# Performance work log

Measured on AMD Instinct MI355X. Metric: run time of the kernel, lower is better.

## Reference

```python
import jax, jax.numpy as jnp
import numpy as np

D_MODEL = 1024; D_STATE = 64; D_CONV = 7; EXPAND = 2; HEADDIM = 64; NGROUPS = 1
D_INNER = EXPAND * D_MODEL            # 2048
NHEADS = D_INNER // HEADDIM           # 32
D_IN_PROJ = 2 * D_INNER + 2 * (2 * NGROUPS * D_STATE) + 2 * NHEADS  # 4416
CONV_DIM = D_INNER + 2 * (2 * NGROUPS * D_STATE)                     # 2304
BATCH = 2; SEQLEN = 2048
EPS = 1e-5


def setup_inputs() -> dict:
    key = jax.random.key(0)
    ks = jax.random.split(key, 8)
    u = jax.random.normal(ks[0], (BATCH, SEQLEN, D_MODEL), jnp.float32)
    W_in = jax.random.normal(ks[1], (D_IN_PROJ, D_MODEL), jnp.float32) * 0.02
    conv_w = jax.random.normal(ks[2], (CONV_DIM, 1, D_CONV), jnp.float32) * 0.2
    conv_b = jax.random.normal(ks[3], (CONV_DIM,), jnp.float32) * 0.02
    # dt_bias init as in module: inv-softplus of dt sampled log-uniform in [dt_min, dt_max]
    dt = jnp.exp(jax.random.uniform(ks[4], (NHEADS,)) * (np.log(0.1) - np.log(0.001)) + np.log(0.001))
    dt = jnp.clip(dt, 1e-4)
    dt_bias = dt + jnp.log(-jnp.expm1(-dt))
    A_log = jnp.zeros((NHEADS,), jnp.float32)          # A = -exp(A_log) = -1
    Dp = jnp.ones((NHEADS,), jnp.float32)
    fc_D_w = jax.random.normal(ks[5], (NHEADS, D_INNER), jnp.float32) * 0.02
    norm_w = jnp.ones((D_INNER,), jnp.float32)
    W_out = jax.random.normal(ks[6], (D_MODEL, D_INNER), jnp.float32) * 0.02
    return dict(u=u, W_in=W_in, conv_w=conv_w, conv_b=conv_b, dt_bias=dt_bias,
                A_log=A_log, Dp=Dp, fc_D_w=fc_D_w, norm_w=norm_w, W_out=W_out)


def reference(u, W_in, conv_w, conv_b, dt_bias, A_log, Dp, fc_D_w, norm_w, W_out):
    b, L, _ = u.shape
    gn = NGROUPS * D_STATE
    zxbcdt = jnp.einsum('bld,ed->ble', u, W_in)              # (b,L,4416)
    A = -jnp.exp(A_log)                                       # (H,)
    z = zxbcdt[..., :D_INNER]
    xBC = zxbcdt[..., D_INNER:D_INNER + CONV_DIM]
    dt_raw = zxbcdt[..., D_INNER + CONV_DIM:]                 # (b,L,2H)
    # fwd dt + time-flipped bwd dt stacked along batch -> (2b,L,H)
    dt = jnp.concatenate([dt_raw[..., :NHEADS], dt_raw[..., NHEADS:][:, ::-1]], axis=0)
    dt = jax.nn.softplus(dt + dt_bias)                        # dt_limit=(0,inf): softplus already >= 0
    # depthwise conv1d, 'same' padding
    xc = jnp.transpose(xBC, (0, 2, 1))                        # (b,Cd,L)
    xc = jax.lax.conv_general_dilated(xc, conv_w, (1,), [(D_CONV // 2, D_CONV // 2)],
                                      dimension_numbers=('NCH', 'OIH', 'NCH'),
                                      feature_group_count=CONV_DIM)
    xc = xc + conv_b[None, :, None]
    xBC = jax.nn.silu(jnp.transpose(xc, (0, 2, 1)))           # (b,L,Cd)
    x = xBC[..., :D_INNER]
    BC = xBC[..., D_INNER:]
    x_og = x
    x2 = jnp.concatenate([x, x[:, ::-1]], axis=0)             # (2b,L,d_inner)
    BC2 = jnp.concatenate([BC[..., :2 * gn], BC[..., 2 * gn:][:, ::-1]], axis=0)
    Bm = BC2[..., :gn].reshape(2 * b, L, NGROUPS, D_STATE)
    Cm = BC2[..., gn:].reshape(2 * b, L, NGROUPS, D_STATE)
    x_scan = x2.reshape(2 * b, L, NHEADS, HEADDIM)
    hpg = NHEADS // NGROUPS
    Bh = jnp.repeat(Bm, hpg, axis=2)                          # (2b,L,H,N)
    Ch = jnp.repeat(Cm, hpg, axis=2)

    def step(state, ins):                                     # state: (2b,H,P,N)
        x_t, dt_t, B_t, C_t = ins
        ex = jnp.exp(A[None, :, None, None] * dt_t[:, :, None, None])
        state = state * ex + x_t[..., None] * B_t[:, :, None, :]
        y_t = jnp.sum(state * C_t[:, :, None, :], axis=-1)    # (2b,H,P)
        return state, y_t

    xs = (jnp.moveaxis(x_scan, 1, 0), jnp.moveaxis(dt, 1, 0),
          jnp.moveaxis(Bh, 1, 0), jnp.moveaxis(Ch, 1, 0))
    state0 = jnp.zeros((2 * b, NHEADS, HEADDIM, D_STATE), u.dtype)
    _, ys = jax.lax.scan(step, state0, xs)                    # (L,2b,H,P)
    y = jnp.moveaxis(ys, 0, 1).reshape(2 * b, L, D_INNER)
    # shift_right: drop last step, zero at t=0
    y = jnp.concatenate([jnp.zeros_like(y[:, :1]), y[:, :-1]], axis=1)
    y_fw, y_bw = y[:b], y[b:][:, ::-1]
    diag_heads = jnp.einsum('bld,hd->blh', x_og, fc_D_w) + Dp # fc_D(x_og) with bias D
    diag = jnp.repeat(diag_heads, HEADDIM, axis=-1)           # expand per-head -> d_inner
    y = y_fw + y_bw + x_og * diag
    # RMSNormGated (norm before gate)
    rms = jnp.sqrt(jnp.mean(y * y, axis=-1, keepdims=True) + EPS)
    y = norm_w * (y / rms) * jax.nn.silu(z)
    return jnp.einsum('ble,de->bld', y, W_out)
```

## Files before the change

### kernel.cpp

```cpp
#include <hip/hip_runtime.h>
#include <cstdint>
#include <cstddef>

#define L_SEQ   2048
#define DMODEL  1024
#define DINNER  2048
#define NHEADS_ 32
#define HEADDIM_ 64
#define DSTATE  64
#define CONVDIM 2304
#define DINPROJ 4416
#define DINPROJ_P 4608
#define BATCH_  2
#define EPS_    1e-5f
#define PITCH   72
#define KSPL    8

typedef __attribute__((ext_vector_type(8))) short bf16x8;
typedef __attribute__((ext_vector_type(4))) float f32x4;
typedef unsigned short ushort_t;
typedef unsigned int uint_t;
typedef __attribute__((address_space(3))) unsigned int as3_uint;
typedef __attribute__((address_space(1))) const unsigned int as1_uint;

__device__ __forceinline__ float silu_f(float v) { return v / (1.f + __expf(-v)); }
__device__ __forceinline__ ushort_t f2bf(float f) {
    uint_t u = __float_as_uint(f);
    return (ushort_t)((u + 0x7FFFu + ((u >> 16) & 1u)) >> 16);
}
__device__ __forceinline__ float bf2f(ushort_t u) {
    return __uint_as_float(((uint_t)u) << 16);
}
__device__ __forceinline__ void gload16(const void* g, void* l) {
    __builtin_amdgcn_global_load_lds((as1_uint*)g, (as3_uint*)l, 16, 0, 0);
}

#define N0U ((size_t)(4096 * 1024 / 4))
#define N1U ((size_t)(DINPROJ_P * DMODEL / 4))
#define N2U ((size_t)(DMODEL * DINNER / 4))
#define N3U ((size_t)(64 * DINNER / 4))
__global__ __launch_bounds__(256)
void cvt_all(const float* __restrict__ u, const float* __restrict__ W_in,
             const float* __restrict__ W_out, const float* __restrict__ fcD,
             ushort_t* __restrict__ ubf, ushort_t* __restrict__ wibf,
             ushort_t* __restrict__ wobf, ushort_t* __restrict__ fcdbf) {
    size_t unit = (size_t)blockIdx.x * 256 + threadIdx.x;
    if (unit >= N0U + N1U + N2U + N3U) return;
    const float* src; ushort_t* dst; size_t i4; bool zero = false;
    if (unit < N0U) {
        i4 = unit; src = u; dst = ubf;
    } else if (unit < N0U + N1U) {
        i4 = unit - N0U; src = W_in; dst = wibf;
        zero = ((int)(i4 / (DMODEL / 4)) >= DINPROJ);
    } else if (unit < N0U + N1U + N2U) {
        i4 = unit - N0U - N1U; src = W_out; dst = wobf;
    } else {
        i4 = unit - N0U - N1U - N2U; src = fcD; dst = fcdbf;
        zero = ((int)(i4 / (DINNER / 4)) >= NHEADS_);
    }
    float4 v = zero ? make_float4(0.f, 0.f, 0.f, 0.f)
                    : reinterpret_cast<const float4*>(src)[i4];
    ushort_t* d = dst + i4 * 4;
    d[0] = f2bf(v.x); d[1] = f2bf(v.y); d[2] = f2bf(v.z); d[3] = f2bf(v.w);
}

__global__ __launch_bounds__(512, 2)
void gemm_8ph(const ushort_t* __restrict__ Ap, const ushort_t* __restrict__ Bp,
              ushort_t* __restrict__ Cbf, int M, int N, int K, int nbn) {
    const int nwg = gridDim.x;
    const int orig = blockIdx.x;
    const int xcd = orig & 7, q_ = nwg >> 3, r_ = nwg & 7;
    const int wg = ((xcd < r_) ? (xcd * (q_ + 1)) : (r_ * (q_ + 1) + (xcd - r_) * q_)) + (orig >> 3);
    const int bm = (wg / nbn) * 256, bn = (wg % nbn) * 256;

    __shared__ __align__(16) char smem[131072];

    const int tid = threadIdx.x;
    const int wave = tid >> 6, lane = tid & 63;
    const int wr = wave >> 2, wc = wave & 3;
    const int fr = lane & 15, kg = lane >> 4, rg = lane >> 4;

    const ushort_t* gptr[8]; uint_t glds[8];
#pragma unroll
    for (int i = 0; i < 8; ++i) {
        int unit = i >> 1, g = i & 1;
        int isB = unit & 1, half = unit >> 1;
        int rbase = half * 128 + wave * 16 + g * 8;
        int rl = rbase + (lane >> 3);
        int slot = (lane & 7) ^ (lane >> 3);
        gptr[i] = (isB ? Bp : Ap) + (size_t)((isB ? bn : bm) + rl) * (size_t)K + slot * 8;
        glds[i] = (uint_t)(isB * 32768 + rbase * 128);
    }
    auto stage = [&](int pbuf, int t) {
#pragma unroll
        for (int i = 0; i < 8; ++i)
            gload16(gptr[i] + (size_t)t * 64, smem + pbuf * 65536 + glds[i]);
    };

    f32x4 acc[8][4];
#pragma unroll
    for (int m = 0; m < 8; ++m)
#pragma unroll
        for (int n = 0; n < 4; ++n) acc[m][n] = (f32x4){0.f, 0.f, 0.f, 0.f};

    bf16x8 aF[4][2];
    bf16x8 bF[2][2][2];

    auto lda_frag = [&](int pbuf, int mh) {
#pragma unroll
        for (int mm = 0; mm < 4; ++mm)
#pragma unroll
            for (int kk = 0; kk < 2; ++kk) {
                int Rl = wr * 128 + mh * 64 + mm * 16 + fr;
                aF[mm][kk] = *reinterpret_cast<const bf16x8*>(
                    smem + pbuf * 65536 + Rl * 128 + (((kk * 4 + kg) ^ (Rl & 7)) << 4));
            }
    };
    auto ldb_frag = [&](int pbuf, int nh) {
#pragma unroll
        for (int nn = 0; nn < 2; ++nn)
#pragma unroll
            for (int kk = 0; kk < 2; ++kk) {
                int Rl = wc * 64 + (nh * 2 + nn) * 16 + fr;
                bF[nh][nn][kk] = *reinterpret_cast<const bf16x8*>(
                    smem + pbuf * 65536 + 32768 + Rl * 128 + (((kk * 4 + kg) ^ (Rl & 7)) << 4));
            }
    };
    auto do_mfma = [&](int mh, int nh) {
        __builtin_amdgcn_s_setprio(1);
#pragma unroll
        for (int mm = 0; mm < 4; ++mm)
#pragma unroll
            for (int nn = 0; nn < 2; ++nn)
#pragma unroll
                for (int kk = 0; kk < 2; ++kk)
                    acc[mh * 4 + mm][nh * 2 + nn] = __builtin_amdgcn_mfma_f32_16x16x32_bf16(
                        aF[mm][kk], bF[nh][nn][kk], acc[mh * 4 + mm][nh * 2 + nn], 0, 0, 0);
        __builtin_amdgcn_s_setprio(0);
    };

    const int NT = K / 64;
    stage(0, 0);
    asm volatile("s_waitcnt vmcnt(0)" ::: "memory");
    __builtin_amdgcn_sched_barrier(0);
    __builtin_amdgcn_s_barrier();

    for (int t = 0; t < NT; ++t) {
        const int p = t & 1;
        if (t + 1 < NT) stage(p ^ 1, t + 1);
        if (t > 0) {
            if (t + 1 < NT) asm volatile("s_waitcnt vmcnt(8)" ::: "memory");
            else            asm volatile("s_waitcnt vmcnt(0)" ::: "memory");
            __builtin_amdgcn_sched_barrier(0);
        }
        __builtin_amdgcn_s_barrier();
        lda_frag(p, 0); ldb_frag(p, 0);
        asm volatile("s_waitcnt lgkmcnt(0)" ::: "memory");
        __builtin_amdgcn_sched_barrier(0);
        do_mfma(0, 0);
        __builtin_amdgcn_s_barrier();
        ldb_frag(p, 1);
        asm volatile("s_waitcnt lgkmcnt(0)" ::: "memory");
        __builtin_amdgcn_sched_barrier(0);
        do_mfma(0, 1);
        __builtin_amdgcn_s_barrier();
        lda_frag(p, 1);
        asm volatile("s_waitcnt lgkmcnt(0)" ::: "memory");
        __builtin_amdgcn_sched_barrier(0);
        do_mfma(1, 0);
        __builtin_amdgcn_s_barrier();
        do_mfma(1, 1);
        __builtin_amdgcn_s_barrier();
    }

    char* ct = smem;
#pragma unroll
    for (int m = 0; m < 8; ++m)
#pragma unroll
        for (int n = 0; n < 4; ++n) {
#pragma unroll
            for (int r = 0; r < 4; ++r) {
                int lr = wr * 128 + m * 16 + rg * 4 + r;
                int lc = wc * 64 + n * 16 + fr;
                int byte = lr * 512 + ((lc * 2) ^ ((lr & 7) << 4));
                *reinterpret_cast<ushort_t*>(ct + byte) = f2bf(acc[m][n][r]);
            }
        }
    __syncthreads();
    for (int pass = 0; pass < 16; ++pass) {
        int unit = pass * 512 + tid;
        int row = unit >> 5, u = unit & 31;
        uint4 v = *reinterpret_cast<const uint4*>(ct + row * 512 + ((u * 16) ^ ((row & 7) << 4)));
        *reinterpret_cast<uint4*>(&Cbf[(size_t)(bm + row) * N + bn + u * 8]) = v;
    }
}

template<int BM, int BN, int WGM, int WGN, int FM, int FN, int MODE>
__global__ __launch_bounds__(256)
void gemm_nt_mfma(const ushort_t* __restrict__ A, const ushort_t* __restrict__ B,
                  float* __restrict__ C, ushort_t* __restrict__ Cbf,
                  int M, int N, int K, int lda, int ldb, int nbn) {
    const int nwg = gridDim.x;
    const int orig = blockIdx.x;
    const int xcd = orig & 7, q = nwg >> 3, r = nwg & 7;
    const int wg = ((xcd < r) ? (xcd * (q + 1)) : (r * (q + 1) + (xcd - r) * q)) + (orig >> 3);

    int bm, bn, kbeg, kend, ks = 0;
    if (MODE == 2) {
        bm = (wg / nbn) * BM; bn = 0; ks = wg % nbn;
        kbeg = ks * (K / nbn); kend = kbeg + K / nbn;
    } else {
        bm = (wg / nbn) * BM; bn = (wg % nbn) * BN;
        kbeg = 0; kend = K;
    }

    constexpr int BUFSZ = (BM + BN) * 64;
    constexpr int EPI_B = (MODE == 2) ? 0 : BM * 256;
    constexpr int SMEM_B = (2 * BUFSZ > EPI_B) ? 2 * BUFSZ : EPI_B;
    __shared__ __align__(16) char smem[SMEM_B];

    const int tid = threadIdx.x;
    const int wave = tid >> 6, lane = tid & 63;
    const int wr = wave / WGN, wc = wave % WGN;
    const int fr = lane & 15, kg = lane >> 4;

    constexpr int AI = BM / 64, BI = BN / 64;
    size_t aoff[AI]; int aLds[AI];
#pragma unroll
    for (int pp = 0; pp < AI; ++pp) {
        int p = wave * AI + pp;
        int row = p * 16 + (lane >> 2);
        int c16 = (lane & 3) ^ ((row >> 1) & 3);
        aoff[pp] = (size_t)(bm + row) * lda + c16 * 8;
        aLds[pp] = p * 1024;
    }
    size_t boff[BI]; int bLds[BI];
#pragma unroll
    for (int pp = 0; pp < BI; ++pp) {
        int p = wave * BI + pp;
        int row = p * 16 + (lane >> 2);
        int c16 = (lane & 3) ^ ((row >> 1) & 3);
        boff[pp] = (size_t)(bn + row) * ldb + c16 * 8;
        bLds[pp] = BM * 64 + p * 1024;
    }

    auto stage = [&](int buf, int k0) {
        char* bp = smem + buf * BUFSZ;
#pragma unroll
        for (int pp = 0; pp < AI; ++pp) gload16(&A[aoff[pp] + k0], bp + aLds[pp]);
#pragma unroll
        for (int pp = 0; pp < BI; ++pp) gload16(&B[boff[pp] + k0], bp + bLds[pp]);
    };

    f32x4 acc[FM][FN];
#pragma unroll
    for (int m = 0; m < FM; ++m)
#pragma unroll
        for (int n = 0; n < FN; ++n) acc[m][n] = (f32x4){0.f, 0.f, 0.f, 0.f};

    stage(0, kbeg);
    __syncthreads();

    const int NT = (kend - kbeg) / 32;
    for (int t = 0; t < NT; ++t) {
        const int cur = t & 1;
        if (t + 1 < NT) stage(cur ^ 1, kbeg + (t + 1) * 32);

        const char* bp = smem + cur * BUFSZ;
        bf16x8 af[FM], bfv[FN];
#pragma unroll
        for (int m = 0; m < FM; ++m) {
            int row = wr * FM * 16 + m * 16 + fr;
            af[m] = *reinterpret_cast<const bf16x8*>(bp + row * 64 + ((kg ^ ((row >> 1) & 3)) << 4));
        }
#pragma unroll
        for (int n = 0; n < FN; ++n) {
            int row = wc * FN * 16 + n * 16 + fr;
            bfv[n] = *reinterpret_cast<const bf16x8*>(bp + BM * 64 + row * 64 + ((kg ^ ((row >> 1) & 3)) << 4));
        }
#pragma unroll
        for (int m = 0; m < FM; ++m)
#pragma unroll
            for (int n = 0; n < FN; ++n)
                acc[m][n] = __builtin_amdgcn_mfma_f32_16x16x32_bf16(af[m], bfv[n], acc[m][n], 0, 0, 0);
        __syncthreads();
    }

    const int rg = lane >> 4;
    if (MODE == 2) {
        float* Cp = C + (size_t)ks * M * NHEADS_;
#pragma unroll
        for (int m = 0; m < FM; ++m)
#pragma unroll
            for (int n = 0; n < FN; ++n) {
                int col = wc * FN * 16 + n * 16 + fr;
#pragma unroll
                for (int r = 0; r < 4; ++r) {
                    int rowg = bm + wr * FM * 16 + m * 16 + rg * 4 + r;
                    if (col < NHEADS_) Cp[(size_t)rowg * NHEADS_ + col] = acc[m][n][r];
                }
            }
    } else {
        char* ct = smem;
#pragma unroll
        for (int m = 0; m < FM; ++m)
#pragma unroll
            for (int n = 0; n < FN; ++n) {
#pragma unroll
                for (int r = 0; r < 4; ++r) {
                    int lr = wr * FM * 16 + m * 16 + rg * 4 + r;
                    int lc = wc * FN * 16 + n * 16 + fr;
                    int byte = (lr * 256 + lc * 4) ^ ((lr & 7) << 4);
                    *reinterpret_cast<float*>(ct + byte) = acc[m][n][r];
                }
            }
        __syncthreads();
        const int lrow = tid >> 4, seg16 = (tid & 15) * 16;
#pragma unroll
        for (int j = 0; j < BM / 16; ++j) {
            int lr = j * 16 + lrow;
            uint4 v = *reinterpret_cast<const uint4*>(ct + ((lr * 256 + seg16) ^ ((lr & 7) << 4)));
            *reinterpret_cast<uint4*>(&C[(size_t)(bm + lr) * N + bn + seg16 / 4]) = v;
        }
    }
}

__global__ __launch_bounds__(256)
void conv_kernel(const ushort_t* __restrict__ zxbf, const float* __restrict__ conv_w,
                 const float* __restrict__ conv_b, ushort_t* __restrict__ xBCbf) {
    const int c = blockIdx.x * 256 + threadIdx.x;
    const int t0 = blockIdx.y * 16;
    const int beta = blockIdx.z;
    float w[7];
#pragma unroll
    for (int k = 0; k < 7; ++k) w[k] = conv_w[c * 7 + k];
    const float bias = conv_b[c];
    const ushort_t* in = zxbf + (size_t)beta * L_SEQ * DINPROJ_P + DINNER + c;
    float win[7];
#pragma unroll
    for (int j = 0; j < 6; ++j) {
        int t = t0 - 3 + j;
        win[j] = (t >= 0 && t < L_SEQ) ? bf2f(in[(size_t)t * DINPROJ_P]) : 0.f;
    }
    for (int i = 0; i < 16; ++i) {
        int t = t0 + i;
        int tl = t + 3;
        win[6] = (tl < L_SEQ) ? bf2f(in[(size_t)tl * DINPROJ_P]) : 0.f;
        float acc = bias;
#pragma unroll
        for (int k = 0; k < 7; ++k) acc += win[k] * w[k];
        xBCbf[((size_t)beta * L_SEQ + t) * CONVDIM + c] = f2bf(silu_f(acc));
#pragma unroll
        for (int j = 0; j < 6; ++j) win[j] = win[j + 1];
    }
}

__global__ __launch_bounds__(256)
void dtla_kernel(const ushort_t* __restrict__ zxbf, const float* __restrict__ dt_bias,
                 const float* __restrict__ A_log, float* __restrict__ labuf) {
    const int idx = blockIdx.x * 256 + threadIdx.x;
    const int h   = idx & 31;
    const int tau = (idx >> 5) & (L_SEQ - 1);
    const int bd  = idx >> 16;
    const int dir = bd >> 1, beta = bd & 1;
    const int tt  = dir ? (L_SEQ - 1 - tau) : tau;
    const float dtraw = bf2f(zxbf[((size_t)beta * L_SEQ + tt) * DINPROJ_P + DINNER + CONVDIM + dir * NHEADS_ + h]);
    const float Ah = -__expf(A_log[h]);
    const float dtv = dtraw + dt_bias[h];
    const float sp = (dtv > 15.f) ? dtv : log1pf(__expf(dtv));
    labuf[((size_t)bd * NHEADS_ + h) * L_SEQ + tau] = Ah * sp;
}

__global__ __launch_bounds__(256)
void ssd_chunk_kernel(const ushort_t* __restrict__ xBCbf, const float* __restrict__ labuf,
                      float* __restrict__ Pbuf, ushort_t* __restrict__ sdel,
                      ushort_t* __restrict__ yfw, ushort_t* __restrict__ ybw) {
    const int c  = blockIdx.x;
    const int h  = blockIdx.y;
    const int bd = blockIdx.z;
    const int dir = bd >> 1, beta = bd & 1;
    const int tid = threadIdx.x;
    const int wave = tid >> 6, lane = tid & 63;
    const int wr = wave >> 1, wc = wave & 1;
    const int fr = lane & 15, kg = lane >> 4, rg = lane >> 4;

    __shared__ short Bs[64 * PITCH], Cs[64 * PITCH], XTs[64 * PITCH],
                     BTs[64 * PITCH], Ms[64 * PITCH];
    __shared__ float lslds[64];

    const int row = tid >> 2, seg = tid & 3;
    const int tau_r = c * 64 + row;
    const int tt = dir ? (L_SEQ - 1 - tau_r) : tau_r;
    const ushort_t* gbase = xBCbf + ((size_t)beta * L_SEQ + tt) * CONVDIM;

    union U4 { uint4 v; ushort_t s[8]; };
    U4 x0, x1, b0, b1, c0, c1;
    x0.v = *reinterpret_cast<const uint4*>(gbase + h * 64 + seg * 16);
    x1.v = *reinterpret_cast<const uint4*>(gbase + h * 64 + seg * 16 + 8);
    b0.v = *reinterpret_cast<const uint4*>(gbase + DINNER + dir * 128 + seg * 16);
    b1.v = *reinterpret_cast<const uint4*>(gbase + DINNER + dir * 128 + seg * 16 + 8);
    c0.v = *reinterpret_cast<const uint4*>(gbase + DINNER + dir * 128 + 64 + seg * 16);
    c1.v = *reinterpret_cast<const uint4*>(gbase + DINNER + dir * 128 + 64 + seg * 16 + 8);

    *reinterpret_cast<uint4*>(&Bs[row * PITCH + seg * 16])     = b0.v;
    *reinterpret_cast<uint4*>(&Bs[row * PITCH + seg * 16 + 8]) = b1.v;
    *reinterpret_cast<uint4*>(&Cs[row * PITCH + seg * 16])     = c0.v;
    *reinterpret_cast<uint4*>(&Cs[row * PITCH + seg * 16 + 8]) = c1.v;
#pragma unroll
    for (int k = 0; k < 8; ++k) {
        XTs[(seg * 16 + k) * PITCH + row]     = x0.s[k];
        XTs[(seg * 16 + 8 + k) * PITCH + row] = x1.s[k];
    }

    if (tid < 64) {
        float v = labuf[((size_t)bd * NHEADS_ + h) * L_SEQ + c * 64 + tid];
#pragma unroll
        for (int d = 1; d < 64; d <<= 1) {
            float t = __shfl_up(v, d);
            if (lane >= d) v += t;
        }
        lslds[tid] = v;
        Pbuf[((size_t)bd * NHEADS_ + h) * L_SEQ + c * 64 + tid] = __expf(v);
    }
    __syncthreads();

    {
        const float wrow = __expf(lslds[63] - lslds[row]);
#pragma unroll
        for (int k = 0; k < 8; ++k) {
            BTs[(seg * 16 + k) * PITCH + row]     = (short)f2bf(bf2f(b0.s[k]) * wrow);
            BTs[(seg * 16 + 8 + k) * PITCH + row] = (short)f2bf(bf2f(b1.s[k]) * wrow);
        }
    }

    f32x4 accg[2][2];
#pragma unroll
    for (int mi = 0; mi < 2; ++mi)
#pragma unroll
        for (int nj = 0; nj < 2; ++nj) accg[mi][nj] = (f32x4){0.f, 0.f, 0.f, 0.f};
#pragma unroll
    for (int s = 0; s < 2; ++s) {
        int koff = kg * 8 + s * 32;
        bf16x8 af[2], bfv[2];
#pragma unroll
        for (int mi = 0; mi < 2; ++mi)
            af[mi] = *reinterpret_cast<const bf16x8*>(&Cs[(wr * 32 + mi * 16 + fr) * PITCH + koff]);
#pragma unroll
        for (int nj = 0; nj < 2; ++nj)
            bfv[nj] = *reinterpret_cast<const bf16x8*>(&Bs[(wc * 32 + nj * 16 + fr) * PITCH + koff]);
#pragma unroll
        for (int mi = 0; mi < 2; ++mi)
#pragma unroll
            for (int nj = 0; nj < 2; ++nj)
                accg[mi][nj] = __builtin_amdgcn_mfma_f32_16x16x32_bf16(af[mi], bfv[nj], accg[mi][nj], 0, 0, 0);
    }

#pragma unroll
    for (int mi = 0; mi < 2; ++mi)
#pragma unroll
        for (int nj = 0; nj < 2; ++nj) {
            int j = wc * 32 + nj * 16 + fr;
            float lsj = lslds[j];
#pragma unroll
            for (int r = 0; r < 4; ++r) {
                int i = wr * 32 + mi * 16 + rg * 4 + r;
                float v = accg[mi][nj][r];
                v = (i >= j) ? v * __expf(lslds[i] - lsj) : 0.f;
                Ms[i * PITCH + j] = (short)f2bf(v);
            }
        }
    __syncthreads();

    f32x4 accy[2][2], accs[2][2];
#pragma unroll
    for (int mi = 0; mi < 2; ++mi)
#pragma unroll
        for (int nj = 0; nj < 2; ++nj) {
            accy[mi][nj] = (f32x4){0.f, 0.f, 0.f, 0.f};
            accs[mi][nj] = (f32x4){0.f, 0.f, 0.f, 0.f};
        }
#pragma unroll
    for (int s = 0; s < 2; ++s) {
        int koff = kg * 8 + s * 32;
        bf16x8 am[2], axt[2], bxt[2], bbt[2];
#pragma unroll
        for (int mi = 0; mi < 2; ++mi) {
            am[mi]  = *reinterpret_cast<const bf16x8*>(&Ms[(wr * 32 + mi * 16 + fr) * PITCH + koff]);
            axt[mi] = *reinterpret_cast<const bf16x8*>(&XTs[(wr * 32 + mi * 16 + fr) * PITCH + koff]);
        }
#pragma unroll
        for (int nj = 0; nj < 2; ++nj) {
            bxt[nj] = *reinterpret_cast<const bf16x8*>(&XTs[(wc * 32 + nj * 16 + fr) * PITCH + koff]);
            bbt[nj] = *reinterpret_cast<const bf16x8*>(&BTs[(wc * 32 + nj * 16 + fr) * PITCH + koff]);
        }
#pragma unroll
        for (int mi = 0; mi < 2; ++mi)
#pragma unroll
            for (int nj = 0; nj < 2; ++nj) {
                accy[mi][nj] = __builtin_amdgcn_mfma_f32_16x16x32_bf16(am[mi], bxt[nj], accy[mi][nj], 0, 0, 0);
                accs[mi][nj] = __builtin_amdgcn_mfma_f32_16x16x32_bf16(axt[mi], bbt[nj], accs[mi][nj], 0, 0, 0);
            }
    }

    ushort_t* Yt = (ushort_t*)Bs;
    ushort_t* St = (ushort_t*)Cs;
#pragma unroll
    for (int mi = 0; mi < 2; ++mi)
#pragma unroll
        for (int nj = 0; nj < 2; ++nj) {
#pragma unroll
            for (int r = 0; r < 4; ++r) {
                int i  = wr * 32 + mi * 16 + rg * 4 + r;
                int jd = wc * 32 + nj * 16 + fr;
                St[i * 64 + jd] = f2bf(accs[mi][nj][r]);
                Yt[i * 64 + jd] = f2bf(accy[mi][nj][r]);
            }
        }
    __syncthreads();

    ushort_t* yout = dir ? ybw : yfw;
    ushort_t* sdp = sdel + (((size_t)bd * NHEADS_ + h) * 32 + c) * 4096;
    for (int un = tid; un < 512; un += 256) {
        const int rowi = un >> 3, ch = un & 7;
        uint4 sv = *reinterpret_cast<const uint4*>(St + rowi * 64 + ch * 8);
        *reinterpret_cast<uint4*>(sdp + rowi * 64 + ch * 8) = sv;
        uint4 yv = *reinterpret_cast<const uint4*>(Yt + rowi * 64 + ch * 8);
        int tau = c * 64 + rowi;
        int tout;
        if (tau == L_SEQ - 1) { tout = dir ? (L_SEQ - 1) : 0; yv = make_uint4(0, 0, 0, 0); }
        else                  { tout = dir ? (L_SEQ - 2 - tau) : (tau + 1); }
        *reinterpret_cast<uint4*>(yout + ((size_t)beta * L_SEQ + tout) * DINNER + h * 64 + ch * 8) = yv;
    }
}

__global__ __launch_bounds__(256)
void ssd_scan_kernel(const float* __restrict__ Pbuf, ushort_t* __restrict__ sdel) {
    const int bh = blockIdx.x;
    const int qt = blockIdx.y;
    const int eo = qt * 1024 + threadIdx.x * 4;
    ushort_t* base = sdel + (size_t)bh * 32 * 4096;
    const float* Pb = Pbuf + (size_t)bh * L_SEQ;

    float S0 = 0.f, S1 = 0.f, S2 = 0.f, S3 = 0.f;
    uint2 d = *reinterpret_cast<const uint2*>(base + eo);
    for (int c = 0; c < 32; ++c) {
        uint2 dn;
        if (c + 1 < 32) dn = *reinterpret_cast<const uint2*>(base + (size_t)(c + 1) * 4096 + eo);
        const float ptot = Pb[c * 64 + 63];
        uint2 pv;
        pv.x = (uint_t)f2bf(S0) | ((uint_t)f2bf(S1) << 16);
        pv.y = (uint_t)f2bf(S2) | ((uint_t)f2bf(S3) << 16);
        *reinterpret_cast<uint2*>(base + (size_t)c * 4096 + eo) = pv;
        S0 = ptot * S0 + bf2f((ushort_t)(d.x & 0xFFFF));
        S1 = ptot * S1 + bf2f((ushort_t)(d.x >> 16));
        S2 = ptot * S2 + bf2f((ushort_t)(d.y & 0xFFFF));
        S3 = ptot * S3 + bf2f((ushort_t)(d.y >> 16));
        d = dn;
    }
}

__global__ __launch_bounds__(256)
void ssd_yinter_kernel(const ushort_t* __restrict__ xBCbf, const float* __restrict__ Pbuf,
                       const ushort_t* __restrict__ sin_buf,
                       ushort_t* __restrict__ yfw, ushort_t* __restrict__ ybw) {
    const int c  = blockIdx.x;
    const int h  = blockIdx.y;
    const int bd = blockIdx.z;
    const int dir = bd >> 1, beta = bd & 1;
    const int tid = threadIdx.x;
    const int wave = tid >> 6, lane = tid & 63;
    const int fr = lane & 15, kg = lane >> 4, rg = lane >> 4;
    const int i0 = wave * 16;

    __shared__ short Cs[64 * PITCH], Ss[64 * PITCH];
    __shared__ float Pl[64];

    const int row = tid >> 2, seg = tid & 3;
    {
        const int tau_r = c * 64 + row;
        const int tt = dir ? (L_SEQ - 1 - tau_r) : tau_r;
        const ushort_t* gbase = xBCbf + ((size_t)beta * L_SEQ + tt) * CONVDIM + DINNER + dir * 128 + 64;
        uint4 cv0 = *reinterpret_cast<const uint4*>(gbase + seg * 16);
        uint4 cv1 = *reinterpret_cast<const uint4*>(gbase + seg * 16 + 8);
        *reinterpret_cast<uint4*>(&Cs[row * PITCH + seg * 16])     = cv0;
        *reinterpret_cast<uint4*>(&Cs[row * PITCH + seg * 16 + 8]) = cv1;
    }
    {
        const ushort_t* sb = sin_buf + (((size_t)bd * NHEADS_ + h) * 32 + c) * 4096;
        for (int un = tid; un < 512; un += 256) {
            const int ri = un >> 3, ch = un & 7;
            uint4 v = *reinterpret_cast<const uint4*>(sb + ri * 64 + ch * 8);
            *reinterpret_cast<uint4*>(&Ss[ri * PITCH + ch * 8]) = v;
        }
    }
    if (tid < 64) Pl[tid] = Pbuf[((size_t)bd * NHEADS_ + h) * L_SEQ + c * 64 + tid];
    __syncthreads();

    f32x4 accy[4];
#pragma unroll
    for (int nf = 0; nf < 4; ++nf) accy[nf] = (f32x4){0.f, 0.f, 0.f, 0.f};
#pragma unroll
    for (int s = 0; s < 2; ++s) {
        int koff = kg * 8 + s * 32;
        bf16x8 af = *reinterpret_cast<const bf16x8*>(&Cs[(i0 + fr) * PITCH + koff]);
#pragma unroll
        for (int nf = 0; nf < 4; ++nf) {
            bf16x8 bfv = *reinterpret_cast<const bf16x8*>(&Ss[(nf * 16 + fr) * PITCH + koff]);
            accy[nf] = __builtin_amdgcn_mfma_f32_16x16x32_bf16(af, bfv, accy[nf], 0, 0, 0);
        }
    }
    __syncthreads();

    ushort_t* Yt = (ushort_t*)Cs;
#pragma unroll
    for (int nf = 0; nf < 4; ++nf) {
        int hdl = nf * 16 + fr;
#pragma unroll
        for (int r = 0; r < 4; ++r) {
            int i = i0 + rg * 4 + r;
            Yt[i * 64 + hdl] = f2bf(accy[nf][r] * Pl[i]);
        }
    }
    __syncthreads();

    ushort_t* yout = dir ? ybw : yfw;
    for (int un = tid; un < 512; un += 256) {
        const int ri = un >> 3, ch = un & 7;
        int tau = c * 64 + ri;
        if (tau == L_SEQ - 1) continue;
        int tout = dir ? (L_SEQ - 2 - tau) : (tau + 1);
        ushort_t* gp = yout + ((size_t)beta * L_SEQ + tout) * DINNER + h * 64 + ch * 8;
        union U4 { uint4 v; ushort_t s[8]; } yo, cv, res;
        yo.v = *reinterpret_cast<const uint4*>(gp);
        cv.v = *reinterpret_cast<const uint4*>(Yt + ri * 64 + ch * 8);
#pragma unroll
        for (int k = 0; k < 8; ++k) res.s[k] = f2bf(bf2f(yo.s[k]) + bf2f(cv.s[k]));
        *reinterpret_cast<uint4*>(gp) = res.v;
    }
}

__global__ __launch_bounds__(256)
void combine_rms(const ushort_t* __restrict__ yfw, const ushort_t* __restrict__ ybw,
                 const ushort_t* __restrict__ xBCbf, const float* __restrict__ dpart,
                 const float* __restrict__ Dp,
                 const ushort_t* __restrict__ zxbf, const float* __restrict__ norm_w,
                 ushort_t* __restrict__ ybf) {
    const int row = blockIdx.x;
    const int tid = threadIdx.x;
    union U4 { uint4 v; ushort_t s[8]; };
    U4 yf, yb, xv, zv;
    yf.v = *reinterpret_cast<const uint4*>(yfw + (size_t)row * DINNER + tid * 8);
    yb.v = *reinterpret_cast<const uint4*>(ybw + (size_t)row * DINNER + tid * 8);
    xv.v = *reinterpret_cast<const uint4*>(xBCbf + (size_t)row * CONVDIM + tid * 8);
    zv.v = *reinterpret_cast<const uint4*>(zxbf + (size_t)row * DINPROJ_P + tid * 8);
    const int hh = tid >> 3;
    float dgv = Dp[hh];
#pragma unroll
    for (int ks = 0; ks < KSPL; ++ks)
        dgv += dpart[((size_t)ks * (BATCH_ * L_SEQ) + row) * NHEADS_ + hh];
    float v[8];
    float ss = 0.f;
#pragma unroll
    for (int i = 0; i < 8; ++i) {
        float val = bf2f(yf.s[i]) + bf2f(yb.s[i]) + bf2f(xv.s[i]) * dgv;
        v[i] = val;
        ss += val * val;
    }
    ss += __shfl_xor(ss, 1);  ss += __shfl_xor(ss, 2);  ss += __shfl_xor(ss, 4);
    ss += __shfl_xor(ss, 8);  ss += __shfl_xor(ss, 16); ss += __shfl_xor(ss, 32);
    __shared__ float wsum[4];
    if ((tid & 63) == 0) wsum[tid >> 6] = ss;
    __syncthreads();
    ss = wsum[0] + wsum[1] + wsum[2] + wsum[3];
    const float inv = rsqrtf(ss * (1.f / DINNER) + EPS_);
    U4 outv;
#pragma unroll
    for (int i = 0; i < 8; ++i) {
        int c = tid * 8 + i;
        outv.s[i] = f2bf(norm_w[c] * v[i] * inv * silu_f(bf2f(zv.s[i])));
    }
    *reinterpret_cast<uint4*>(ybf + (size_t)row * DINNER + tid * 8) = outv.v;
}

extern "C" void kernel_launch(void* const* d_in, const int* in_sizes, int n_in,
                              void* d_out, int out_size, void* d_ws, size_t ws_size,
                              hipStream_t stream) {
    const float* u       = (const float*)d_in[0];
    const float* W_in    = (const float*)d_in[1];
    const float* conv_w  = (const float*)d_in[2];
    const float* conv_b  = (const float*)d_in[3];
    const float* dt_bias = (const float*)d_in[4];
    const float* A_log   = (const float*)d_in[5];
    const float* Dp      = (const float*)d_in[6];
    const float* fc_D_w  = (const float*)d_in[7];
    const float* norm_w  = (const float*)d_in[8];
    const float* W_out   = (const float*)d_in[9];
    float* out = (float*)d_out;

    const int ROWS = BATCH_ * L_SEQ;
    ushort_t* zxbf  = (ushort_t*)d_ws;
    ushort_t* xBCbf = zxbf  + (size_t)ROWS * DINPROJ_P;
    ushort_t* yfw   = xBCbf + (size_t)ROWS * CONVDIM;
    ushort_t* ybw   = yfw   + (size_t)ROWS * DINNER;
    float* dpart = (float*)(ybw + (size_t)ROWS * DINNER);
    float* labuf = dpart + (size_t)KSPL * ROWS * NHEADS_;
    float* Pbuf  = labuf + (size_t)4 * NHEADS_ * L_SEQ;
    ushort_t* sdel = (ushort_t*)(Pbuf + (size_t)4 * NHEADS_ * L_SEQ);
    ushort_t* wobf = sdel + (size_t)4 * NHEADS_ * 32 * 64 * 64;
    ushort_t* fcdbf = wobf + (size_t)DMODEL * DINNER;
    ushort_t* ubf  = fcdbf + (size_t)64 * DINNER;
    ushort_t* wibf = ubf  + (size_t)ROWS * DMODEL;
    ushort_t* ybf  = ubf;

    const size_t total_units = N0U + N1U + N2U + N3U;
    cvt_all<<<(int)((total_units + 255) / 256), 256, 0, stream>>>(
        u, W_in, W_out, fc_D_w, ubf, wibf, wobf, fcdbf);

    gemm_8ph<<<(ROWS / 256) * (DINPROJ_P / 256), 512, 0, stream>>>(
        ubf, wibf, zxbf, ROWS, DINPROJ_P, DMODEL, DINPROJ_P / 256);

    dim3 gc(CONVDIM / 256, L_SEQ / 16, BATCH_);
    conv_kernel<<<gc, 256, 0, stream>>>(zxbf, conv_w, conv_b, xBCbf);

    dtla_kernel<<<(4 * L_SEQ * NHEADS_) / 256, 256, 0, stream>>>(zxbf, dt_bias, A_log, labuf);

    dim3 ga(32, NHEADS_, 4);
    ssd_chunk_kernel<<<ga, 256, 0, stream>>>(xBCbf, labuf, Pbuf, sdel, yfw, ybw);

    dim3 gsn(4 * NHEADS_, 4);
    ssd_scan_kernel<<<gsn, 256, 0, stream>>>(Pbuf, sdel);

    dim3 gy(32, NHEADS_, 4);
    ssd_yinter_kernel<<<gy, 256, 0, stream>>>(xBCbf, Pbuf, sdel, yfw, ybw);

    gemm_nt_mfma<64, 64, 2, 2, 2, 2, 2><<<(ROWS / 64) * KSPL, 256, 0, stream>>>(
        xBCbf, fcdbf, dpart, nullptr, ROWS, 64, DINNER, CONVDIM, DINNER, KSPL);

    combine_rms<<<ROWS, 256, 0, stream>>>(yfw, ybw, xBCbf, dpart, Dp, zxbf, norm_w, ybf);

    gemm_nt_mfma<128, 64, 2, 2, 4, 2, 0><<<(ROWS / 128) * (DMODEL / 64), 256, 0, stream>>>(
        ybf, wobf, out, nullptr, ROWS, DMODEL, DINNER, DINNER, DINNER, DMODEL / 64);
}
```

Measured before the change: 219.6 us.

## Interleave half-tile global loads with MFMA phases in the bf16 GEMM

Replaces the whole-tile prefetch at the top of each K iteration with finer-grained half-tile loads (A/B halves) spread across the four MFMA sub-phases. The loop is unrolled by two over the double buffer, and a half-buffer is refilled as soon as its fragments have been consumed. The aim is to keep global-to-LDS traffic continuously overlapped with compute and to reduce stalls at the waitcnt points. The cost is more complex vmcnt bookkeeping, which depends on NT being even, and a risk of LDS read/write hazards if the stage order is wrong.

Measured after the change: 214.4 us. 2.4% less time.

```diff
diff --git a/kernel.cpp b/kernel.cpp
--- a/kernel.cpp
+++ b/kernel.cpp
@@ -79,22 +79,19 @@
     const int wave = tid >> 6, lane = tid & 63;
     const int wr = wave >> 2, wc = wave & 3;
     const int fr = lane & 15, kg = lane >> 4, rg = lane >> 4;
-
-    const ushort_t* gptr[8]; uint_t glds[8];
-#pragma unroll
-    for (int i = 0; i < 8; ++i) {
-        int unit = i >> 1, g = i & 1;
-        int isB = unit & 1, half = unit >> 1;
-        int rbase = half * 128 + wave * 16 + g * 8;
-        int rl = rbase + (lane >> 3);
-        int slot = (lane & 7) ^ (lane >> 3);
-        gptr[i] = (isB ? Bp : Ap) + (size_t)((isB ? bn : bm) + rl) * (size_t)K + slot * 8;
-        glds[i] = (uint_t)(isB * 32768 + rbase * 128);
-    }
-    auto stage = [&](int pbuf, int t) {
-#pragma unroll
-        for (int i = 0; i < 8; ++i)
-            gload16(gptr[i] + (size_t)t * 64, smem + pbuf * 65536 + glds[i]);
+    const int NT = K / 64;
+
+    const int rA = lane >> 3;
+    const int slot = (lane & 7) ^ rA;
+    auto stage_half = [&](int pbuf, int isB, int half, int t) {
+        if (t >= NT) return;
+#pragma unroll
+        for (int g = 0; g < 2; ++g) {
+            int rbase = half * 128 + wave * 16 + g * 8;
+            const ushort_t* src = (isB ? Bp : Ap)
+                + (size_t)((isB ? bn : bm) + rbase + rA) * (size_t)K + slot * 8 + (size_t)t * 64;
+            gload16(src, smem + pbuf * 65536 + isB * 32768 + rbase * 128);
+        }
     };
 
     f32x4 acc[8][4];
@@ -139,39 +136,72 @@
         __builtin_amdgcn_s_setprio(0);
     };
 
-    const int NT = K / 64;
-    stage(0, 0);
+    stage_half(0, 0, 0, 0); stage_half(0, 1, 0, 0);
+    stage_half(0, 0, 1, 0); stage_half(0, 1, 1, 0);
+    stage_half(1, 0, 0, 1); stage_half(1, 1, 0, 1);
     asm volatile("s_waitcnt vmcnt(0)" ::: "memory");
     __builtin_amdgcn_sched_barrier(0);
     __builtin_amdgcn_s_barrier();
 
-    for (int t = 0; t < NT; ++t) {
-        const int p = t & 1;
-        if (t + 1 < NT) stage(p ^ 1, t + 1);
-        if (t > 0) {
-            if (t + 1 < NT) asm volatile("s_waitcnt vmcnt(8)" ::: "memory");
-            else            asm volatile("s_waitcnt vmcnt(0)" ::: "memory");
-            __builtin_amdgcn_sched_barrier(0);
-        }
-        __builtin_amdgcn_s_barrier();
-        lda_frag(p, 0); ldb_frag(p, 0);
+    const int NITER = NT / 2;
+    for (int j = 0; j < NITER; ++j) {
+        const int o = 2 * j + 1, e2 = 2 * j + 2, o2 = 2 * j + 3;
+        stage_half(1, 0, 1, o);
+        asm volatile("s_waitcnt vmcnt(6)" ::: "memory");
+        __builtin_amdgcn_sched_barrier(0);
+        __builtin_amdgcn_s_barrier();
+        lda_frag(0, 0); ldb_frag(0, 0);
         asm volatile("s_waitcnt lgkmcnt(0)" ::: "memory");
         __builtin_amdgcn_sched_barrier(0);
         do_mfma(0, 0);
         __builtin_amdgcn_s_barrier();
-        ldb_frag(p, 1);
+        stage_half(1, 1, 1, o);
+        ldb_frag(0, 1);
         asm volatile("s_waitcnt lgkmcnt(0)" ::: "memory");
         __builtin_amdgcn_sched_barrier(0);
         do_mfma(0, 1);
         __builtin_amdgcn_s_barrier();
-        lda_frag(p, 1);
+        stage_half(0, 1, 0, e2);
+        lda_frag(0, 1);
         asm volatile("s_waitcnt lgkmcnt(0)" ::: "memory");
         __builtin_amdgcn_sched_barrier(0);
         do_mfma(1, 0);
         __builtin_amdgcn_s_barrier();
+        stage_half(0, 0, 0, e2);
         do_mfma(1, 1);
         __builtin_amdgcn_s_barrier();
-    }
+        stage_half(0, 0, 1, e2);
+        if (e2 < NT) {
+            asm volatile("s_waitcnt vmcnt(6)" ::: "memory");
+        } else {
+            asm volatile("s_waitcnt vmcnt(0)" ::: "memory");
+        }
+        __builtin_amdgcn_sched_barrier(0);
+        __builtin_amdgcn_s_barrier();
+        lda_frag(1, 0); ldb_frag(1, 0);
+        asm volatile("s_waitcnt lgkmcnt(0)" ::: "memory");
+        __builtin_amdgcn_sched_barrier(0);
+        do_mfma(0, 0);
+        __builtin_amdgcn_s_barrier();
+        stage_half(0, 1, 1, e2);
+        ldb_frag(1, 1);
+        asm volatile("s_waitcnt lgkmcnt(0)" ::: "memory");
+        __builtin_amdgcn_sched_barrier(0);
+        do_mfma(0, 1);
+        __builtin_amdgcn_s_barrier();
+        stage_half(1, 1, 0, o2);
+        lda_frag(1, 1);
+        asm volatile("s_waitcnt lgkmcnt(0)" ::: "memory");
+        __builtin_amdgcn_sched_barrier(0);
+        do_mfma(1, 0);
+        __builtin_amdgcn_s_barrier();
+        stage_half(1, 0, 0, o2);
+        do_mfma(1, 1);
+        __builtin_amdgcn_s_barrier();
+    }
+    asm volatile("s_waitcnt vmcnt(0)" ::: "memory");
+    __builtin_amdgcn_sched_barrier(0);
+    __builtin_amdgcn_s_barrier();
 
     char* ct = smem;
 #pragma unroll
```
